# Optimization experiments

Hardware: AMD Instinct MI355X
Metric: run time of the kernel (lower is better)

Reference implementation:

```python
import jax, jax.numpy as jnp
import numpy as np
from jax import lax

B, D_IN, L = 32, 128, 2048
D_STATE = 512


def setup_inputs() -> dict:
    key = jax.random.key(0)
    ks = jax.random.split(key, 7)
    s_in = 1.0 / np.sqrt(D_STATE)
    return {
        "x": jax.random.normal(ks[0], (B, D_IN, L), dtype=jnp.float32),
        "W_ih": jax.random.normal(ks[1], (D_STATE, D_IN), dtype=jnp.float32) * s_in,
        "W_hh": jax.random.normal(ks[2], (D_STATE, D_STATE), dtype=jnp.float32) * s_in,
        "b_ih": jax.random.normal(ks[3], (D_STATE,), dtype=jnp.float32) * s_in,
        "b_hh": jax.random.normal(ks[4], (D_STATE,), dtype=jnp.float32) * s_in,
        "W_fc": jax.random.normal(ks[5], (D_IN, D_STATE), dtype=jnp.float32) * s_in,
        "b_fc": jax.random.normal(ks[6], (D_IN,), dtype=jnp.float32) * s_in,
    }


def reference(x, W_ih, W_hh, b_ih, b_hh, W_fc, b_fc):
    # x: [B, d_input, L] -> [L, B, d_input] (matches x.permute(2,0,1))
    xs = jnp.transpose(x, (2, 0, 1))
    L_, B_ = xs.shape[0], xs.shape[1]
    d_state = W_hh.shape[0]
    d_out = W_fc.shape[0]
    # precompute input projection for all timesteps: [L, B, d_state]
    pre = jnp.einsum('lbd,hd->lbh', xs, W_ih) + b_ih + b_hh

    def step(h, p):
        # h_t = tanh(W_ih x_t + b_ih + W_hh h_{t-1} + b_hh)
        h_new = jnp.tanh(p + h @ W_hh.T)
        return h_new, h_new

    h0 = jnp.zeros((B_, d_state), dtype=x.dtype)
    _, hs = lax.scan(step, h0, pre)  # hs: [L, B, d_state]

    h_flat = hs.reshape(-1, d_state)              # [L*B, d_state]
    y = jnp.tanh(h_flat @ W_fc.T + b_fc)          # [L*B, d_out]
    y = y.reshape(-1, d_out, L_)                  # matches torch reshape(-1, d_output, L)
    return y
```

## Files before the change

### kernel.cpp

```cpp
#include <hip/hip_runtime.h>
#include <cstdint>

typedef _Float16 half_t;
typedef __attribute__((ext_vector_type(2))) _Float16 half2_t;
typedef __attribute__((ext_vector_type(4))) _Float16 half4_t;
typedef __attribute__((ext_vector_type(8))) _Float16 half8_t;
typedef __attribute__((ext_vector_type(4))) float f32x4;

#define B_    32
#define DIN   128
#define LEN   2048
#define DS    512
#define NKT   16
#define KTR   12
#define KTL   (NKT - KTR)
#define LDSB_BYTES (KTL * 32 * 1024)
#define HBUF_OFF   LDSB_BYTES
#define LDS_BYTES  (LDSB_BYTES + 2 * DS * 2)

__device__ __forceinline__ float fast_tanh(float x) {
    float e = __expf(2.0f * x);
    return 1.0f - 2.0f / (e + 1.0f);
}

__device__ __forceinline__ float fd2(uint32_t a, uint32_t b, float c) {
    return __builtin_amdgcn_fdot2(__builtin_bit_cast(half2_t, a),
                                  __builtin_bit_cast(half2_t, b), c, false);
}

__device__ __forceinline__ half8_t load_wfrag(const float* __restrict__ W,
                                              int n0, int c, int q, int kt) {
    const float* p = W + (size_t)(n0 + c) * DS + kt * 32 + q * 8;
    float4 f0 = *(const float4*)p;
    float4 f1 = *(const float4*)(p + 4);
    half8_t r = {(half_t)f0.x, (half_t)f0.y, (half_t)f0.z, (half_t)f0.w,
                 (half_t)f1.x, (half_t)f1.y, (half_t)f1.z, (half_t)f1.w};
    return r;
}

__global__ __launch_bounds__(256) void rnn_pre_kernel(
    const float* __restrict__ x, const float* __restrict__ Wih,
    const float* __restrict__ bih, const float* __restrict__ bhh,
    half_t* __restrict__ pre)
{
    __shared__ half_t Xs[64 * 136];
    __shared__ half_t Ws[128 * 136];
    const int t  = threadIdx.x;
    const int l0 = blockIdx.x * 64;
    const int b  = blockIdx.y;
    const int h0 = blockIdx.z * 128;

#pragma unroll
    for (int i = 0; i < 32; ++i) {
        int idx = i * 256 + t;
        int j = idx & 63, d = idx >> 6;
        Xs[j * 136 + d] = (half_t)x[(size_t)b * DIN * LEN + (size_t)d * LEN + l0 + j];
    }
#pragma unroll
    for (int i = 0; i < 16; ++i) {
        int f4 = i * 256 + t;
        int h = f4 >> 5, d4 = f4 & 31;
        float4 w = *(const float4*)&Wih[(size_t)(h0 + h) * DIN + d4 * 4];
        half4_t hw = {(half_t)w.x, (half_t)w.y, (half_t)w.z, (half_t)w.w};
        *(half4_t*)&Ws[h * 136 + d4 * 4] = hw;
    }
    __syncthreads();

    const int lb = (t >> 4) * 4;
    const int hb = (t & 15) * 8;
    float acc[4][8];
#pragma unroll
    for (int i = 0; i < 4; ++i)
#pragma unroll
        for (int j = 0; j < 8; ++j) acc[i][j] = 0.f;

    for (int kc = 0; kc < DIN; kc += 8) {
        uint4 xa[4], wb[8];
#pragma unroll
        for (int i = 0; i < 4; ++i) xa[i] = *(const uint4*)&Xs[(lb + i) * 136 + kc];
#pragma unroll
        for (int j = 0; j < 8; ++j) wb[j] = *(const uint4*)&Ws[(hb + j) * 136 + kc];
#pragma unroll
        for (int i = 0; i < 4; ++i)
#pragma unroll
            for (int j = 0; j < 8; ++j) {
                float a = acc[i][j];
                a = fd2(xa[i].x, wb[j].x, a);
                a = fd2(xa[i].y, wb[j].y, a);
                a = fd2(xa[i].z, wb[j].z, a);
                a = fd2(xa[i].w, wb[j].w, a);
                acc[i][j] = a;
            }
    }

    float bias[8];
#pragma unroll
    for (int j = 0; j < 8; ++j) bias[j] = bih[h0 + hb + j] + bhh[h0 + hb + j];
#pragma unroll
    for (int i = 0; i < 4; ++i) {
        half8_t s;
#pragma unroll
        for (int j = 0; j < 8; ++j) s[j] = (half_t)(acc[i][j] + bias[j]);
        *(half8_t*)&pre[((size_t)b * LEN + l0 + lb + i) * DS + h0 + hb] = s;
    }
}

__global__ __launch_bounds__(512) __attribute__((amdgpu_waves_per_eu(2, 2)))
void rnn_recur_kernel(
    const float* __restrict__ Whh, const half_t* __restrict__ pre,
    half_t* __restrict__ hs)
{
    extern __shared__ char smem[];
    const int t    = threadIdx.x;
    const int b    = blockIdx.x;
    const int w    = t >> 6;
    const int lane = t & 63;
    const int c    = lane & 15;
    const int q    = lane >> 4;
    const int n0w  = w * 64;

    half8_t breg[KTR][4];
#pragma unroll
    for (int kt = 0; kt < KTR; ++kt)
#pragma unroll
        for (int nt = 0; nt < 4; ++nt)
            breg[kt][nt] = load_wfrag(Whh, n0w + nt * 16, c, q, kt);

#pragma unroll
    for (int kt = KTR; kt < NKT; ++kt)
#pragma unroll
        for (int nt = 0; nt < 4; ++nt) {
            half8_t f = load_wfrag(Whh, n0w + nt * 16, c, q, kt);
            int gid = w * 4 + nt;
            *(half8_t*)(smem + (((kt - KTR) * 32 + gid) << 10) + lane * 16) = f;
        }
    if (t < DS) *(half_t*)(smem + HBUF_OFF + t * 2) = (half_t)0.f;
    __syncthreads();

    const half_t* prew = pre + (size_t)b * LEN * DS + n0w + lane;
    half_t* hsb = hs + (size_t)b * DS;
    float pv0 = (float)prew[0];
    float pv1 = (float)prew[DS];

    int par = 0;
    for (int l = 0; l < LEN; ++l) {
        int l2 = (l + 2 < LEN) ? (l + 2) : (LEN - 1);
        float pv2 = (float)prew[(size_t)l2 * DS];

        const char* hb = smem + HBUF_OFF + par * 1024;
        f32x4 acc0 = {0.f, 0.f, 0.f, 0.f};
        f32x4 acc1 = {0.f, 0.f, 0.f, 0.f};
        f32x4 acc2 = {0.f, 0.f, 0.f, 0.f};
        f32x4 acc3 = {0.f, 0.f, 0.f, 0.f};
#pragma unroll
        for (int kt = 0; kt < KTR; ++kt) {
            half8_t a = *(const half8_t*)(hb + kt * 64 + q * 16);
            acc0 = __builtin_amdgcn_mfma_f32_16x16x32_f16(a, breg[kt][0], acc0, 0, 0, 0);
            acc1 = __builtin_amdgcn_mfma_f32_16x16x32_f16(a, breg[kt][1], acc1, 0, 0, 0);
            acc2 = __builtin_amdgcn_mfma_f32_16x16x32_f16(a, breg[kt][2], acc2, 0, 0, 0);
            acc3 = __builtin_amdgcn_mfma_f32_16x16x32_f16(a, breg[kt][3], acc3, 0, 0, 0);
        }
#pragma unroll
        for (int kt = KTR; kt < NKT; ++kt) {
            half8_t a = *(const half8_t*)(hb + kt * 64 + q * 16);
            const char* bb = smem + (((kt - KTR) * 32 + w * 4) << 10) + lane * 16;
            half8_t b0 = *(const half8_t*)(bb);
            half8_t b1 = *(const half8_t*)(bb + 1024);
            half8_t b2 = *(const half8_t*)(bb + 2048);
            half8_t b3 = *(const half8_t*)(bb + 3072);
            acc0 = __builtin_amdgcn_mfma_f32_16x16x32_f16(a, b0, acc0, 0, 0, 0);
            acc1 = __builtin_amdgcn_mfma_f32_16x16x32_f16(a, b1, acc1, 0, 0, 0);
            acc2 = __builtin_amdgcn_mfma_f32_16x16x32_f16(a, b2, acc2, 0, 0, 0);
            acc3 = __builtin_amdgcn_mfma_f32_16x16x32_f16(a, b3, acc3, 0, 0, 0);
        }

        float a01 = (q & 1) ? acc1.x : acc0.x;
        float a23 = (q & 1) ? acc3.x : acc2.x;
        float av  = (q & 2) ? a23 : a01;
        half_t hv = (half_t)fast_tanh(pv0 + av);

        char* hn = smem + HBUF_OFF + (par ^ 1) * 1024;
        *(half_t*)(hn + (n0w + lane) * 2) = hv;
        hsb[(size_t)l * (B_ * DS) + n0w + lane] = hv;

        pv0 = pv1;
        pv1 = pv2;
        par ^= 1;
        asm volatile("s_waitcnt lgkmcnt(0)\n\ts_barrier" ::: "memory");
    }
}

__global__ __launch_bounds__(256) void rnn_out_kernel(
    const half_t* __restrict__ hs, const float* __restrict__ Wfc,
    const float* __restrict__ bfc, float* __restrict__ y)
{
    __shared__ half_t Hs[64 * 72];
    __shared__ half_t Ws[128 * 72];
    const int t  = threadIdx.x;
    const int r0 = blockIdx.x * 64;

    const int lb = (t >> 4) * 4;
    const int ob = (t & 15) * 8;
    float acc[4][8];
#pragma unroll
    for (int i = 0; i < 4; ++i)
#pragma unroll
        for (int j = 0; j < 8; ++j) acc[i][j] = 0.f;

    for (int kc = 0; kc < DS; kc += 64) {
#pragma unroll
        for (int i = 0; i < 2; ++i) {
            int u = i * 256 + t;
            int r = u >> 3, c8 = u & 7;
            uint4 v = ((const uint4*)(hs + (size_t)(r0 + r) * DS + kc))[c8];
            *(uint4*)&Hs[r * 72 + c8 * 8] = v;
        }
#pragma unroll
        for (int i = 0; i < 8; ++i) {
            int u = i * 256 + t;
            int o = u >> 4, c4 = u & 15;
            float4 wv = *(const float4*)&Wfc[(size_t)o * DS + kc + c4 * 4];
            half4_t hw = {(half_t)wv.x, (half_t)wv.y, (half_t)wv.z, (half_t)wv.w};
            *(half4_t*)&Ws[o * 72 + c4 * 4] = hw;
        }
        __syncthreads();
#pragma unroll
        for (int k8 = 0; k8 < 64; k8 += 8) {
            uint4 xa[4], wb[8];
#pragma unroll
            for (int i = 0; i < 4; ++i) xa[i] = *(const uint4*)&Hs[(lb + i) * 72 + k8];
#pragma unroll
            for (int j = 0; j < 8; ++j) wb[j] = *(const uint4*)&Ws[(ob + j) * 72 + k8];
#pragma unroll
            for (int i = 0; i < 4; ++i)
#pragma unroll
                for (int j = 0; j < 8; ++j) {
                    float a = acc[i][j];
                    a = fd2(xa[i].x, wb[j].x, a);
                    a = fd2(xa[i].y, wb[j].y, a);
                    a = fd2(xa[i].z, wb[j].z, a);
                    a = fd2(xa[i].w, wb[j].w, a);
                    acc[i][j] = a;
                }
        }
        __syncthreads();
    }

#pragma unroll
    for (int i = 0; i < 4; ++i) {
        float4 r0v = {fast_tanh(acc[i][0] + bfc[ob + 0]), fast_tanh(acc[i][1] + bfc[ob + 1]),
                      fast_tanh(acc[i][2] + bfc[ob + 2]), fast_tanh(acc[i][3] + bfc[ob + 3])};
        float4 r1v = {fast_tanh(acc[i][4] + bfc[ob + 4]), fast_tanh(acc[i][5] + bfc[ob + 5]),
                      fast_tanh(acc[i][6] + bfc[ob + 6]), fast_tanh(acc[i][7] + bfc[ob + 7])};
        float* yr = y + (size_t)(r0 + lb + i) * DIN + ob;
        *(float4*)yr       = r0v;
        *((float4*)yr + 1) = r1v;
    }
}

extern "C" void kernel_launch(void* const* d_in, const int* in_sizes, int n_in,
                              void* d_out, int out_size, void* d_ws, size_t ws_size,
                              hipStream_t stream) {
    (void)in_sizes; (void)n_in; (void)out_size; (void)ws_size;
    const float* x   = (const float*)d_in[0];
    const float* Wih = (const float*)d_in[1];
    const float* Whh = (const float*)d_in[2];
    const float* bih = (const float*)d_in[3];
    const float* bhh = (const float*)d_in[4];
    const float* Wfc = (const float*)d_in[5];
    const float* bfc = (const float*)d_in[6];
    float* y = (float*)d_out;

    half_t* pre = (half_t*)d_ws;
    half_t* hs  = (half_t*)((char*)d_ws + (size_t)B_ * LEN * DS * 2);

    hipFuncSetAttribute((const void*)rnn_recur_kernel,
                        hipFuncAttributeMaxDynamicSharedMemorySize, LDS_BYTES);

    rnn_pre_kernel<<<dim3(LEN / 64, B_, DS / 128), 256, 0, stream>>>(x, Wih, bih, bhh, pre);
    rnn_recur_kernel<<<dim3(B_), 512, LDS_BYTES, stream>>>(Whh, pre, hs);
    rnn_out_kernel<<<dim3(LEN * B_ / 64), 256, 0, stream>>>(hs, Wfc, bfc, y);
}
```

Before: 2.980 ms.

## Stream the spilled W_hh tiles from a global fp16 scratch instead of LDS

A new pre-kernel converts the last four k-tiles of W_hh to fp16 in the MFMA fragment layout. It writes them into a scratch region at the tail of the output buffer. The recurrence kernel no longer keeps these tiles in dynamic LDS; it reloads them from global memory (via L1/L2) every timestep, and LDS is left holding only the h double buffer. The aim is to cut LDS footprint and LDS read traffic per step. The cost is cache-latency loads on the serial critical path, and the scratch relies on the output tail only being overwritten after the recurrence finishes.

```diff
diff --git a/kernel.cpp b/kernel.cpp
--- a/kernel.cpp
+++ b/kernel.cpp
@@ -14,9 +14,7 @@
 #define NKT   16
 #define KTR   12
 #define KTL   (NKT - KTR)
-#define LDSB_BYTES (KTL * 32 * 1024)
-#define HBUF_OFF   LDSB_BYTES
-#define LDS_BYTES  (LDSB_BYTES + 2 * DS * 2)
+#define WSCR_BYTES (KTL * 32 * 1024)
 
 __device__ __forceinline__ float fast_tanh(float x) {
     float e = __expf(2.0f * x);
@@ -105,12 +103,28 @@
     }
 }
 
+__global__ __launch_bounds__(256) void rnn_wconv_kernel(
+    const float* __restrict__ Whh, half_t* __restrict__ wscr)
+{
+    const int t = blockIdx.x * 256 + threadIdx.x;
+    const int lane = t & 63;
+    const int gid  = (t >> 6) & 31;
+    const int ktp  = t >> 11;
+    const int c = lane & 15, q = lane >> 4;
+    const float* p = Whh + (size_t)(gid * 16 + c) * DS + (KTR + ktp) * 32 + q * 8;
+    float4 f0 = *(const float4*)p;
+    float4 f1 = *(const float4*)(p + 4);
+    half8_t r = {(half_t)f0.x, (half_t)f0.y, (half_t)f0.z, (half_t)f0.w,
+                 (half_t)f1.x, (half_t)f1.y, (half_t)f1.z, (half_t)f1.w};
+    *(half8_t*)&wscr[(size_t)t * 8] = r;
+}
+
 __global__ __launch_bounds__(512) __attribute__((amdgpu_waves_per_eu(2, 2)))
 void rnn_recur_kernel(
     const float* __restrict__ Whh, const half_t* __restrict__ pre,
-    half_t* __restrict__ hs)
-{
-    extern __shared__ char smem[];
+    half_t* __restrict__ hs, const half_t* __restrict__ wscr)
+{
+    __shared__ half_t hbuf[2][DS];
     const int t    = threadIdx.x;
     const int b    = blockIdx.x;
     const int w    = t >> 6;
@@ -126,16 +140,10 @@
         for (int nt = 0; nt < 4; ++nt)
             breg[kt][nt] = load_wfrag(Whh, n0w + nt * 16, c, q, kt);
 
-#pragma unroll
-    for (int kt = KTR; kt < NKT; ++kt)
-#pragma unroll
-        for (int nt = 0; nt < 4; ++nt) {
-            half8_t f = load_wfrag(Whh, n0w + nt * 16, c, q, kt);
-            int gid = w * 4 + nt;
-            *(half8_t*)(smem + (((kt - KTR) * 32 + gid) << 10) + lane * 16) = f;
-        }
-    if (t < DS) *(half_t*)(smem + HBUF_OFF + t * 2) = (half_t)0.f;
+    if (t < DS) hbuf[0][t] = (half_t)0.f;
     __syncthreads();
+
+    const char* wsb = (const char*)wscr + (w << 12) + lane * 16;
 
     const half_t* prew = pre + (size_t)b * LEN * DS + n0w + lane;
     half_t* hsb = hs + (size_t)b * DS;
@@ -147,7 +155,14 @@
         int l2 = (l + 2 < LEN) ? (l + 2) : (LEN - 1);
         float pv2 = (float)prew[(size_t)l2 * DS];
 
-        const char* hb = smem + HBUF_OFF + par * 1024;
+        half8_t bg[KTL][4];
+#pragma unroll
+        for (int ktp = 0; ktp < KTL; ++ktp)
+#pragma unroll
+            for (int nt = 0; nt < 4; ++nt)
+                bg[ktp][nt] = *(const half8_t*)(wsb + (((ktp * 32) + nt) << 10));
+
+        const char* hb = (const char*)&hbuf[par][0];
         f32x4 acc0 = {0.f, 0.f, 0.f, 0.f};
         f32x4 acc1 = {0.f, 0.f, 0.f, 0.f};
         f32x4 acc2 = {0.f, 0.f, 0.f, 0.f};
@@ -161,17 +176,12 @@
             acc3 = __builtin_amdgcn_mfma_f32_16x16x32_f16(a, breg[kt][3], acc3, 0, 0, 0);
         }
 #pragma unroll
-        for (int kt = KTR; kt < NKT; ++kt) {
-            half8_t a = *(const half8_t*)(hb + kt * 64 + q * 16);
-            const char* bb = smem + (((kt - KTR) * 32 + w * 4) << 10) + lane * 16;
-            half8_t b0 = *(const half8_t*)(bb);
-            half8_t b1 = *(const half8_t*)(bb + 1024);
-            half8_t b2 = *(const half8_t*)(bb + 2048);
-            half8_t b3 = *(const half8_t*)(bb + 3072);
-            acc0 = __builtin_amdgcn_mfma_f32_16x16x32_f16(a, b0, acc0, 0, 0, 0);
-            acc1 = __builtin_amdgcn_mfma_f32_16x16x32_f16(a, b1, acc1, 0, 0, 0);
-            acc2 = __builtin_amdgcn_mfma_f32_16x16x32_f16(a, b2, acc2, 0, 0, 0);
-            acc3 = __builtin_amdgcn_mfma_f32_16x16x32_f16(a, b3, acc3, 0, 0, 0);
+        for (int ktp = 0; ktp < KTL; ++ktp) {
+            half8_t a = *(const half8_t*)(hb + (KTR + ktp) * 64 + q * 16);
+            acc0 = __builtin_amdgcn_mfma_f32_16x16x32_f16(a, bg[ktp][0], acc0, 0, 0, 0);
+            acc1 = __builtin_amdgcn_mfma_f32_16x16x32_f16(a, bg[ktp][1], acc1, 0, 0, 0);
+            acc2 = __builtin_amdgcn_mfma_f32_16x16x32_f16(a, bg[ktp][2], acc2, 0, 0, 0);
+            acc3 = __builtin_amdgcn_mfma_f32_16x16x32_f16(a, bg[ktp][3], acc3, 0, 0, 0);
         }
 
         float a01 = (q & 1) ? acc1.x : acc0.x;
@@ -179,8 +189,7 @@
         float av  = (q & 2) ? a23 : a01;
         half_t hv = (half_t)fast_tanh(pv0 + av);
 
-        char* hn = smem + HBUF_OFF + (par ^ 1) * 1024;
-        *(half_t*)(hn + (n0w + lane) * 2) = hv;
+        hbuf[par ^ 1][n0w + lane] = hv;
         hsb[(size_t)l * (B_ * DS) + n0w + lane] = hv;
 
         pv0 = pv1;
@@ -261,7 +270,7 @@
 extern "C" void kernel_launch(void* const* d_in, const int* in_sizes, int n_in,
                               void* d_out, int out_size, void* d_ws, size_t ws_size,
                               hipStream_t stream) {
-    (void)in_sizes; (void)n_in; (void)out_size; (void)ws_size;
+    (void)in_sizes; (void)n_in; (void)ws_size;
     const float* x   = (const float*)d_in[0];
     const float* Wih = (const float*)d_in[1];
     const float* Whh = (const float*)d_in[2];
@@ -274,10 +283,10 @@
     half_t* pre = (half_t*)d_ws;
     half_t* hs  = (half_t*)((char*)d_ws + (size_t)B_ * LEN * DS * 2);
 
-    hipFuncSetAttribute((const void*)rnn_recur_kernel,
-                        hipFuncAttributeMaxDynamicSharedMemorySize, LDS_BYTES);
-
+    half_t* wscr = (half_t*)((char*)d_out + (size_t)out_size - WSCR_BYTES);
+
+    rnn_wconv_kernel<<<dim3(WSCR_BYTES / 16 / 256), 256, 0, stream>>>(Whh, wscr);
     rnn_pre_kernel<<<dim3(LEN / 64, B_, DS / 128), 256, 0, stream>>>(x, Wih, bih, bhh, pre);
-    rnn_recur_kernel<<<dim3(B_), 512, LDS_BYTES, stream>>>(Whh, pre, hs);
+    rnn_recur_kernel<<<dim3(B_), 512, 0, stream>>>(Whh, pre, hs, wscr);
     rnn_out_kernel<<<dim3(LEN * B_ / 64), 256, 0, stream>>>(hs, Wfc, bfc, y);
 }
```

Measured after the change: 6.615 ms. +122.0%, slower.

## Stream last W_hh k-tile from global scratch in fp16 instead of LDS

Applied to the files above, without the earlier changes.

The last of the four LDS-resident W_hh k-tiles is moved out of LDS. A new kernel pre-converts it to fp16 MFMA fragment order, and the recurrence loop reloads it from global memory (expected to hit cache) every timestep. This cuts LDS traffic and the LDS footprint per step at the cost of extra global loads, placed behind a scheduling barrier. The scratch buffer sits in the tail of the output buffer, which rnn_out_kernel then overwrites. The pre and hs pointer arithmetic is also simplified to incremented pointers.

```diff
diff --git a/kernel.cpp b/kernel.cpp
--- a/kernel.cpp
+++ b/kernel.cpp
@@ -13,10 +13,12 @@
 #define DS    512
 #define NKT   16
 #define KTR   12
-#define KTL   (NKT - KTR)
-#define LDSB_BYTES (KTL * 32 * 1024)
+#define KTLL  3
+#define KTG_KT 15
+#define LDSB_BYTES (KTLL * 32 * 1024)
 #define HBUF_OFF   LDSB_BYTES
 #define LDS_BYTES  (LDSB_BYTES + 2 * DS * 2)
+#define WSCR_BYTES (32 * 1024)
 
 __device__ __forceinline__ float fast_tanh(float x) {
     float e = __expf(2.0f * x);
@@ -105,10 +107,25 @@
     }
 }
 
+__global__ __launch_bounds__(256) void rnn_wconv_kernel(
+    const float* __restrict__ Whh, half_t* __restrict__ wscr)
+{
+    const int t = blockIdx.x * 256 + threadIdx.x;
+    const int lane = t & 63;
+    const int gid  = t >> 6;
+    const int c = lane & 15, q = lane >> 4;
+    const float* p = Whh + (size_t)(gid * 16 + c) * DS + KTG_KT * 32 + q * 8;
+    float4 f0 = *(const float4*)p;
+    float4 f1 = *(const float4*)(p + 4);
+    half8_t r = {(half_t)f0.x, (half_t)f0.y, (half_t)f0.z, (half_t)f0.w,
+                 (half_t)f1.x, (half_t)f1.y, (half_t)f1.z, (half_t)f1.w};
+    *(half8_t*)&wscr[(size_t)t * 8] = r;
+}
+
 __global__ __launch_bounds__(512) __attribute__((amdgpu_waves_per_eu(2, 2)))
 void rnn_recur_kernel(
     const float* __restrict__ Whh, const half_t* __restrict__ pre,
-    half_t* __restrict__ hs)
+    half_t* __restrict__ hs, const half_t* __restrict__ wscr)
 {
     extern __shared__ char smem[];
     const int t    = threadIdx.x;
@@ -127,7 +144,7 @@
             breg[kt][nt] = load_wfrag(Whh, n0w + nt * 16, c, q, kt);
 
 #pragma unroll
-    for (int kt = KTR; kt < NKT; ++kt)
+    for (int kt = KTR; kt < KTR + KTLL; ++kt)
 #pragma unroll
         for (int nt = 0; nt < 4; ++nt) {
             half8_t f = load_wfrag(Whh, n0w + nt * 16, c, q, kt);
@@ -137,15 +154,24 @@
     if (t < DS) *(half_t*)(smem + HBUF_OFF + t * 2) = (half_t)0.f;
     __syncthreads();
 
+    const char* wsb = (const char*)wscr + (w << 12) + lane * 16;
+
     const half_t* prew = pre + (size_t)b * LEN * DS + n0w + lane;
-    half_t* hsb = hs + (size_t)b * DS;
     float pv0 = (float)prew[0];
     float pv1 = (float)prew[DS];
+    const half_t* pw2 = prew + 2 * (size_t)DS;
+    half_t* hw = hs + (size_t)b * DS;
 
     int par = 0;
     for (int l = 0; l < LEN; ++l) {
-        int l2 = (l + 2 < LEN) ? (l + 2) : (LEN - 1);
-        float pv2 = (float)prew[(size_t)l2 * DS];
+        half8_t bg0 = *(const half8_t*)(wsb);
+        half8_t bg1 = *(const half8_t*)(wsb + 1024);
+        half8_t bg2 = *(const half8_t*)(wsb + 2048);
+        half8_t bg3 = *(const half8_t*)(wsb + 3072);
+        __builtin_amdgcn_sched_barrier(0);
+
+        float pv2 = (float)*pw2;
+        if (l < LEN - 3) pw2 += DS;
 
         const char* hb = smem + HBUF_OFF + par * 1024;
         f32x4 acc0 = {0.f, 0.f, 0.f, 0.f};
@@ -161,9 +187,9 @@
             acc3 = __builtin_amdgcn_mfma_f32_16x16x32_f16(a, breg[kt][3], acc3, 0, 0, 0);
         }
 #pragma unroll
-        for (int kt = KTR; kt < NKT; ++kt) {
-            half8_t a = *(const half8_t*)(hb + kt * 64 + q * 16);
-            const char* bb = smem + (((kt - KTR) * 32 + w * 4) << 10) + lane * 16;
+        for (int ktp = 0; ktp < KTLL; ++ktp) {
+            half8_t a = *(const half8_t*)(hb + (KTR + ktp) * 64 + q * 16);
+            const char* bb = smem + ((ktp * 32 + w * 4) << 10) + lane * 16;
             half8_t b0 = *(const half8_t*)(bb);
             half8_t b1 = *(const half8_t*)(bb + 1024);
             half8_t b2 = *(const half8_t*)(bb + 2048);
@@ -173,6 +199,13 @@
             acc2 = __builtin_amdgcn_mfma_f32_16x16x32_f16(a, b2, acc2, 0, 0, 0);
             acc3 = __builtin_amdgcn_mfma_f32_16x16x32_f16(a, b3, acc3, 0, 0, 0);
         }
+        {
+            half8_t a = *(const half8_t*)(hb + KTG_KT * 64 + q * 16);
+            acc0 = __builtin_amdgcn_mfma_f32_16x16x32_f16(a, bg0, acc0, 0, 0, 0);
+            acc1 = __builtin_amdgcn_mfma_f32_16x16x32_f16(a, bg1, acc1, 0, 0, 0);
+            acc2 = __builtin_amdgcn_mfma_f32_16x16x32_f16(a, bg2, acc2, 0, 0, 0);
+            acc3 = __builtin_amdgcn_mfma_f32_16x16x32_f16(a, bg3, acc3, 0, 0, 0);
+        }
 
         float a01 = (q & 1) ? acc1.x : acc0.x;
         float a23 = (q & 1) ? acc3.x : acc2.x;
@@ -181,7 +214,8 @@
 
         char* hn = smem + HBUF_OFF + (par ^ 1) * 1024;
         *(half_t*)(hn + (n0w + lane) * 2) = hv;
-        hsb[(size_t)l * (B_ * DS) + n0w + lane] = hv;
+        hw[n0w + lane] = hv;
+        hw += B_ * DS;
 
         pv0 = pv1;
         pv1 = pv2;
@@ -261,7 +295,7 @@
 extern "C" void kernel_launch(void* const* d_in, const int* in_sizes, int n_in,
                               void* d_out, int out_size, void* d_ws, size_t ws_size,
                               hipStream_t stream) {
-    (void)in_sizes; (void)n_in; (void)out_size; (void)ws_size;
+    (void)in_sizes; (void)n_in; (void)ws_size;
     const float* x   = (const float*)d_in[0];
     const float* Wih = (const float*)d_in[1];
     const float* Whh = (const float*)d_in[2];
@@ -274,10 +308,13 @@
     half_t* pre = (half_t*)d_ws;
     half_t* hs  = (half_t*)((char*)d_ws + (size_t)B_ * LEN * DS * 2);
 
+    half_t* wscr = (half_t*)((char*)d_out + (size_t)out_size - WSCR_BYTES);
+
     hipFuncSetAttribute((const void*)rnn_recur_kernel,
                         hipFuncAttributeMaxDynamicSharedMemorySize, LDS_BYTES);
 
+    rnn_wconv_kernel<<<dim3(WSCR_BYTES / 16 / 256), 256, 0, stream>>>(Whh, wscr);
     rnn_pre_kernel<<<dim3(LEN / 64, B_, DS / 128), 256, 0, stream>>>(x, Wih, bih, bhh, pre);
-    rnn_recur_kernel<<<dim3(B_), 512, LDS_BYTES, stream>>>(Whh, pre, hs);
+    rnn_recur_kernel<<<dim3(B_), 512, LDS_BYTES, stream>>>(Whh, pre, hs, wscr);
     rnn_out_kernel<<<dim3(LEN * B_ / 64), 256, 0, stream>>>(hs, Wfc, bfc, y);
 }
```

Result: slower. 3.374 ms (+13.2%).

## Rotate K-tile order per wave and start next step's MFMAs before barrier

Applied to the files above, without the earlier changes.

Each wave now processes K tiles in a rotated order starting at its own output slice, so the first two K tiles of the next step consume only h values this wave just produced. Those two tiles' MFMAs are issued right after writing h, before the block barrier, overlapping part of the next step's matrix work with barrier wait. It also replaces per-step index arithmetic with pointer increments. This adds complexity in fragment ordering and relies on each wave reading only its own writes before the barrier, which depends on the lgkmcnt wait and same-wave LDS ordering.

```diff
diff --git a/kernel.cpp b/kernel.cpp
--- a/kernel.cpp
+++ b/kernel.cpp
@@ -121,49 +121,55 @@
 
     half8_t breg[KTR][4];
 #pragma unroll
-    for (int kt = 0; kt < KTR; ++kt)
+    for (int j = 0; j < KTR; ++j)
 #pragma unroll
         for (int nt = 0; nt < 4; ++nt)
-            breg[kt][nt] = load_wfrag(Whh, n0w + nt * 16, c, q, kt);
-
-#pragma unroll
-    for (int kt = KTR; kt < NKT; ++kt)
+            breg[j][nt] = load_wfrag(Whh, n0w + nt * 16, c, q, (2 * w + j) & 15);
+
+#pragma unroll
+    for (int j = KTR; j < NKT; ++j)
 #pragma unroll
         for (int nt = 0; nt < 4; ++nt) {
-            half8_t f = load_wfrag(Whh, n0w + nt * 16, c, q, kt);
-            int gid = w * 4 + nt;
-            *(half8_t*)(smem + (((kt - KTR) * 32 + gid) << 10) + lane * 16) = f;
+            half8_t f = load_wfrag(Whh, n0w + nt * 16, c, q, (2 * w + j) & 15);
+            int slot = (j - KTR) * 32 + w * 4 + nt;
+            *(half8_t*)(smem + (slot << 10) + lane * 16) = f;
         }
     if (t < DS) *(half_t*)(smem + HBUF_OFF + t * 2) = (half_t)0.f;
     __syncthreads();
 
     const half_t* prew = pre + (size_t)b * LEN * DS + n0w + lane;
-    half_t* hsb = hs + (size_t)b * DS;
     float pv0 = (float)prew[0];
     float pv1 = (float)prew[DS];
+    const half_t* pw2 = prew + 2 * (size_t)DS;
+    half_t* hw = hs + (size_t)b * DS;
+
+    const int wq16 = w * 128 + q * 16;
+
+    f32x4 acc0 = {0.f, 0.f, 0.f, 0.f};
+    f32x4 acc1 = {0.f, 0.f, 0.f, 0.f};
+    f32x4 acc2 = {0.f, 0.f, 0.f, 0.f};
+    f32x4 acc3 = {0.f, 0.f, 0.f, 0.f};
 
     int par = 0;
     for (int l = 0; l < LEN; ++l) {
-        int l2 = (l + 2 < LEN) ? (l + 2) : (LEN - 1);
-        float pv2 = (float)prew[(size_t)l2 * DS];
+        float pv2 = (float)*pw2;
+        if (l < LEN - 3) pw2 += DS;
 
         const char* hb = smem + HBUF_OFF + par * 1024;
-        f32x4 acc0 = {0.f, 0.f, 0.f, 0.f};
-        f32x4 acc1 = {0.f, 0.f, 0.f, 0.f};
-        f32x4 acc2 = {0.f, 0.f, 0.f, 0.f};
-        f32x4 acc3 = {0.f, 0.f, 0.f, 0.f};
-#pragma unroll
-        for (int kt = 0; kt < KTR; ++kt) {
-            half8_t a = *(const half8_t*)(hb + kt * 64 + q * 16);
-            acc0 = __builtin_amdgcn_mfma_f32_16x16x32_f16(a, breg[kt][0], acc0, 0, 0, 0);
-            acc1 = __builtin_amdgcn_mfma_f32_16x16x32_f16(a, breg[kt][1], acc1, 0, 0, 0);
-            acc2 = __builtin_amdgcn_mfma_f32_16x16x32_f16(a, breg[kt][2], acc2, 0, 0, 0);
-            acc3 = __builtin_amdgcn_mfma_f32_16x16x32_f16(a, breg[kt][3], acc3, 0, 0, 0);
-        }
-#pragma unroll
-        for (int kt = KTR; kt < NKT; ++kt) {
-            half8_t a = *(const half8_t*)(hb + kt * 64 + q * 16);
-            const char* bb = smem + (((kt - KTR) * 32 + w * 4) << 10) + lane * 16;
+#pragma unroll
+        for (int j = 2; j < KTR; ++j) {
+            int off = (w * 128 + j * 64) & 1023;
+            half8_t a = *(const half8_t*)(hb + off + q * 16);
+            acc0 = __builtin_amdgcn_mfma_f32_16x16x32_f16(a, breg[j][0], acc0, 0, 0, 0);
+            acc1 = __builtin_amdgcn_mfma_f32_16x16x32_f16(a, breg[j][1], acc1, 0, 0, 0);
+            acc2 = __builtin_amdgcn_mfma_f32_16x16x32_f16(a, breg[j][2], acc2, 0, 0, 0);
+            acc3 = __builtin_amdgcn_mfma_f32_16x16x32_f16(a, breg[j][3], acc3, 0, 0, 0);
+        }
+#pragma unroll
+        for (int j = KTR; j < NKT; ++j) {
+            int off = (w * 128 + j * 64) & 1023;
+            half8_t a = *(const half8_t*)(hb + off + q * 16);
+            const char* bb = smem + (((j - KTR) * 32 + w * 4) << 10) + lane * 16;
             half8_t b0 = *(const half8_t*)(bb);
             half8_t b1 = *(const half8_t*)(bb + 1024);
             half8_t b2 = *(const half8_t*)(bb + 2048);
@@ -181,7 +187,26 @@
 
         char* hn = smem + HBUF_OFF + (par ^ 1) * 1024;
         *(half_t*)(hn + (n0w + lane) * 2) = hv;
-        hsb[(size_t)l * (B_ * DS) + n0w + lane] = hv;
+        hw[n0w + lane] = hv;
+        hw += B_ * DS;
+
+        acc0 = (f32x4){0.f, 0.f, 0.f, 0.f};
+        acc1 = (f32x4){0.f, 0.f, 0.f, 0.f};
+        acc2 = (f32x4){0.f, 0.f, 0.f, 0.f};
+        acc3 = (f32x4){0.f, 0.f, 0.f, 0.f};
+        if (l != LEN - 1) {
+            half8_t a0 = *(const half8_t*)(hn + wq16);
+            half8_t a1 = *(const half8_t*)(hn + wq16 + 64);
+            acc0 = __builtin_amdgcn_mfma_f32_16x16x32_f16(a0, breg[0][0], acc0, 0, 0, 0);
+            acc1 = __builtin_amdgcn_mfma_f32_16x16x32_f16(a0, breg[0][1], acc1, 0, 0, 0);
+            acc2 = __builtin_amdgcn_mfma_f32_16x16x32_f16(a0, breg[0][2], acc2, 0, 0, 0);
+            acc3 = __builtin_amdgcn_mfma_f32_16x16x32_f16(a0, breg[0][3], acc3, 0, 0, 0);
+            acc0 = __builtin_amdgcn_mfma_f32_16x16x32_f16(a1, breg[1][0], acc0, 0, 0, 0);
+            acc1 = __builtin_amdgcn_mfma_f32_16x16x32_f16(a1, breg[1][1], acc1, 0, 0, 0);
+            acc2 = __builtin_amdgcn_mfma_f32_16x16x32_f16(a1, breg[1][2], acc2, 0, 0, 0);
+            acc3 = __builtin_amdgcn_mfma_f32_16x16x32_f16(a1, breg[1][3], acc3, 0, 0, 0);
+            __builtin_amdgcn_sched_barrier(0);
+        }
 
         pv0 = pv1;
         pv1 = pv2;
```

Result: slower. 3.409 ms (+14.4%).
